# Kernel optimization log

Hardware: AMD Instinct MI355X
Metric: run time of the kernel (lower is better)

The kernel has to match this reference:

```python
import jax, jax.numpy as jnp
import numpy as np

N = 200_000
E = 3_200_000
H = 24

def setup_inputs() -> dict:
    key = jax.random.key(0)
    ks = jax.random.split(key, 12)
    s = 1.0 / np.sqrt(H).astype(np.float32)
    u = lambda k, shape: jax.random.uniform(k, shape, jnp.float32, -s, s)
    return {
        "x": jax.random.normal(ks[0], (N,), jnp.float32),
        "h0": jax.random.normal(ks[1], (1, N, H), jnp.float32) * 0.1,
        "c0": jax.random.normal(ks[2], (1, N, H), jnp.float32) * 0.1,
        "edge_index": jax.random.randint(ks[3], (2, E), 0, N, dtype=jnp.int32),
        "w_ih": u(ks[4], (4 * H, 1)),
        "w_hh": u(ks[5], (4 * H, H)),
        "b_ih": u(ks[6], (4 * H,)),
        "b_hh": u(ks[7], (4 * H,)),
        "gcn_w": u(ks[8], (H, H)),
        "gcn_b": u(ks[9], (H,)),
        "lin_w": u(ks[10], (1, H)),
        "lin_b": u(ks[11], (1,)),
    }

def reference(x, h0, c0, edge_index, w_ih, w_hh, b_ih, b_hh, gcn_w, gcn_b, lin_w, lin_b):
    # --- LSTM single step (seq_len=1, batch=N, input_size=1, hidden=H) ---
    h_prev = h0[0]  # [N, H]
    c_prev = c0[0]  # [N, H]
    # gates in torch order: input, forget, cell(g), output
    gates = x[:, None] * w_ih[:, 0][None, :] + b_ih + h_prev @ w_hh.T + b_hh  # [N, 4H]
    i, f, g, o = jnp.split(gates, 4, axis=-1)
    i = jax.nn.sigmoid(i); f = jax.nn.sigmoid(f); o = jax.nn.sigmoid(o); g = jnp.tanh(g)
    c = f * c_prev + i * g
    h = o * jnp.tanh(c)  # [N, H] -- LSTM output == new hidden state

    # --- GCNConv(24,24): symmetric norm with self loops (PyG default) ---
    xw = h @ gcn_w.T  # [N, H]
    src, dst = edge_index[0], edge_index[1]
    deg = jax.ops.segment_sum(jnp.ones(src.shape, xw.dtype), dst, num_segments=N) + 1.0
    dinv = jax.lax.rsqrt(deg)                      # deg >= 1 due to self loops
    norm = dinv[src] * dinv[dst]                   # [E]
    msg = xw[src] * norm[:, None]                  # [E, H]
    agg = jax.ops.segment_sum(msg, dst, num_segments=N)
    agg = agg + xw * (dinv * dinv)[:, None]        # self-loop edges
    conv = agg + gcn_b                             # [N, H]

    # --- Linear(24,1) + elementwise gate ---
    out = (conv @ lin_w.T + lin_b).reshape(-1)     # [N]
    return x * out, h[None], c[None]
```

## Files before the change

kernel.cpp:

```cpp
#include <hip/hip_runtime.h>
#include <math.h>

#define H 24
#define B0 4096
#define B0_SHIFT 12
#define MAXNB 64
#define NBPAD 65
#define P 20
#define CAP 70000
#define CSTRIDE 16
#define K1_EPB 4096

__device__ __forceinline__ float sigmoidf_(float v) {
    return 1.0f / (1.0f + __expf(-v));
}
__device__ __forceinline__ float tanhf_(float v) {
    return 1.0f - 2.0f / (__expf(2.0f * v) + 1.0f);
}

__global__ void init_kernel(unsigned* __restrict__ cursors,
                            const float* __restrict__ gcn_w,
                            const float* __restrict__ gcn_b,
                            const float* __restrict__ lin_w,
                            const float* __restrict__ lin_b,
                            float* __restrict__ g, float* __restrict__ cb, int NB) {
    int t = threadIdx.x;
    if (t < H) {
        float acc = 0.0f;
        for (int j = 0; j < H; j++) acc = fmaf(lin_w[j], gcn_w[j * H + t], acc);
        g[t] = acc;
    }
    if (t == 32) {
        float c = lin_b[0];
        for (int j = 0; j < H; j++) c = fmaf(gcn_b[j], lin_w[j], c);
        *cb = c;
    }
    if (t < MAXNB) cursors[t * CSTRIDE] = (unsigned)t * CAP;
}

__global__ __launch_bounds__(256) void scatter_kernel(
    const int* __restrict__ src, const int* __restrict__ dst,
    unsigned* __restrict__ cursors, unsigned* __restrict__ pedge, int E, int NB)
{
    __shared__ unsigned cnt[4][NBPAD];
    __shared__ unsigned c3[4][NBPAD];
    __shared__ unsigned base[4][NBPAD];

    const int tid = threadIdx.x;
    const int w = tid >> 6;
    const int start = blockIdx.x * K1_EPB;
    const bool full = (E - start) >= K1_EPB;
    const int ebase = start + tid * 16;

    for (int i = tid; i < 4 * NBPAD; i += 256) {
        (&cnt[0][0])[i] = 0;
        (&c3[0][0])[i] = 0;
    }
    __syncthreads();

    unsigned dreg[16];
    if (full) {
        const uint4* dp = (const uint4*)(dst + ebase);
        #pragma unroll
        for (int q = 0; q < 4; q++) {
            uint4 v = dp[q];
            dreg[4*q+0] = v.x; dreg[4*q+1] = v.y; dreg[4*q+2] = v.z; dreg[4*q+3] = v.w;
        }
        #pragma unroll
        for (int q = 0; q < 16; q++)
            atomicAdd(&cnt[w][dreg[q] >> B0_SHIFT], 1u);
    } else {
        #pragma unroll
        for (int q = 0; q < 16; q++) {
            int e = ebase + q;
            if (e < E) {
                unsigned d = (unsigned)dst[e];
                dreg[q] = d;
                atomicAdd(&cnt[w][d >> B0_SHIFT], 1u);
            } else dreg[q] = 0xFFFFFFFFu;
        }
    }
    __syncthreads();

    if (tid < NB) {
        unsigned c0 = cnt[0][tid], c1 = cnt[1][tid], c2 = cnt[2][tid], cw3 = cnt[3][tid];
        unsigned tot = c0 + c1 + c2 + cw3;
        unsigned gb = tot ? atomicAdd(&cursors[tid * CSTRIDE], tot) : 0u;
        base[0][tid] = gb;
        base[1][tid] = gb + c0;
        base[2][tid] = gb + c0 + c1;
        base[3][tid] = gb + c0 + c1 + c2;
    }
    __syncthreads();

    if (full) {
        unsigned sreg[16];
        const uint4* sp = (const uint4*)(src + ebase);
        #pragma unroll
        for (int q = 0; q < 4; q++) {
            uint4 v = sp[q];
            sreg[4*q+0] = v.x; sreg[4*q+1] = v.y; sreg[4*q+2] = v.z; sreg[4*q+3] = v.w;
        }
        #pragma unroll
        for (int q = 0; q < 16; q++) {
            unsigned d = dreg[q];
            unsigned b = d >> B0_SHIFT;
            unsigned slot = atomicAdd(&c3[w][b], 1u);
            unsigned idx  = base[w][b] + slot;
            if (idx < (b + 1u) * CAP)
                pedge[idx] = (sreg[q] << B0_SHIFT) | (d & (B0 - 1));
        }
    } else {
        #pragma unroll
        for (int q = 0; q < 16; q++) {
            int e = ebase + q;
            if (e < E) {
                unsigned d = dreg[q];
                unsigned b = d >> B0_SHIFT;
                unsigned slot = atomicAdd(&c3[w][b], 1u);
                unsigned idx  = base[w][b] + slot;
                if (idx < (b + 1u) * CAP)
                    pedge[idx] = ((unsigned)src[e] << B0_SHIFT) | (d & (B0 - 1));
            }
        }
    }
}

__global__ __launch_bounds__(256) void deghist_kernel(
    const unsigned* __restrict__ pedge, const unsigned* __restrict__ cursors,
    unsigned short* __restrict__ degp, int NB, int NPAD)
{
    __shared__ unsigned h[B0];
    int b = blockIdx.x % NB, p = blockIdx.x / NB;
    for (int i = threadIdx.x; i < B0; i += 256) h[i] = 0;
    __syncthreads();
    unsigned base = (unsigned)b * CAP;
    unsigned sz = cursors[b * CSTRIDE] - base; if (sz > CAP) sz = CAP;
    unsigned chunk = (sz + P - 1) / P;
    unsigned s0 = p * chunk;
    unsigned s1 = s0 + chunk; if (s1 > sz) s1 = sz;
    for (unsigned i = s0 + threadIdx.x; i < s1; i += 256)
        atomicAdd(&h[pedge[base + i] & (B0 - 1)], 1u);
    __syncthreads();
    unsigned short* out = degp + (size_t)p * NPAD + (size_t)b * B0;
    for (int i = threadIdx.x; i < B0; i += 256) out[i] = (unsigned short)h[i];
}

__global__ __launch_bounds__(256) void node_kernel(
    const float* __restrict__ x, const float* __restrict__ h0, const float* __restrict__ c0,
    const float* __restrict__ w_ih, const float* __restrict__ w_hh,
    const float* __restrict__ b_ih, const float* __restrict__ b_hh,
    const float* __restrict__ g,
    float* __restrict__ out_h, float* __restrict__ out_c,
    float* __restrict__ y, int N)
{
    __shared__ float ws[96 * 24];
    __shared__ float swih[96];
    __shared__ float sbs[96];
    __shared__ float sg[24];

    #pragma unroll 3
    for (int i = threadIdx.x; i < 96 * 24; i += 256) ws[i] = w_hh[i];
    if (threadIdx.x < 96) {
        swih[threadIdx.x] = w_ih[threadIdx.x];
        sbs[threadIdx.x]  = b_ih[threadIdx.x] + b_hh[threadIdx.x];
    } else if (threadIdx.x >= 128 && threadIdx.x < 152) {
        sg[threadIdx.x - 128] = g[threadIdx.x - 128];
    }
    __syncthreads();

    int tid = blockIdx.x * 256 + threadIdx.x;
    int pr  = tid >> 2;
    int n0  = pr * 2;
    if (n0 >= N) return;
    int n1  = n0 + 1;
    int t   = tid & 3;
    int k0  = 6 * t;

    float hp0[H], hp1[H];
    {
        const float4* a4 = (const float4*)(h0 + (size_t)n0 * H);
        const float4* b4 = (const float4*)(h0 + (size_t)n1 * H);
        #pragma unroll
        for (int q = 0; q < 6; q++) {
            float4 va = a4[q], vb = b4[q];
            hp0[4*q+0] = va.x; hp0[4*q+1] = va.y; hp0[4*q+2] = va.z; hp0[4*q+3] = va.w;
            hp1[4*q+0] = vb.x; hp1[4*q+1] = vb.y; hp1[4*q+2] = vb.z; hp1[4*q+3] = vb.w;
        }
    }
    float cp0[6], cp1[6];
    {
        const float2* a2 = (const float2*)(c0 + (size_t)n0 * H + k0);
        const float2* b2 = (const float2*)(c0 + (size_t)n1 * H + k0);
        #pragma unroll
        for (int q = 0; q < 3; q++) {
            float2 va = a2[q], vb = b2[q];
            cp0[2*q] = va.x; cp0[2*q+1] = va.y;
            cp1[2*q] = vb.x; cp1[2*q+1] = vb.y;
        }
    }
    float xv0 = x[n0], xv1 = x[n1];
    float yv0 = 0.0f, yv1 = 0.0f;

    #pragma unroll
    for (int i = 0; i < 6; i++) {
        int k = k0 + i;
        float bi = sbs[k], bf = sbs[k + 24], bg = sbs[k + 48], bo = sbs[k + 72];
        float wik = swih[k], wfk = swih[k + 24], wgk = swih[k + 48], wok = swih[k + 72];
        float gi0 = fmaf(xv0, wik, bi), gi1 = fmaf(xv1, wik, bi);
        float gf0 = fmaf(xv0, wfk, bf), gf1 = fmaf(xv1, wfk, bf);
        float gg0 = fmaf(xv0, wgk, bg), gg1 = fmaf(xv1, wgk, bg);
        float go0 = fmaf(xv0, wok, bo), go1 = fmaf(xv1, wok, bo);
        const float* w0 = ws + k * 24;
        #pragma unroll
        for (int c = 0; c < 6; c++) {
            float4 wi = *(const float4*)(w0 + 4*c);
            float4 wf = *(const float4*)(w0 + 576  + 4*c);
            float4 wg = *(const float4*)(w0 + 1152 + 4*c);
            float4 wo = *(const float4*)(w0 + 1728 + 4*c);
            float a0 = hp0[4*c+0], a1 = hp0[4*c+1], a2 = hp0[4*c+2], a3 = hp0[4*c+3];
            float d0 = hp1[4*c+0], d1 = hp1[4*c+1], d2 = hp1[4*c+2], d3 = hp1[4*c+3];
            gi0 = fmaf(a0, wi.x, gi0); gi0 = fmaf(a1, wi.y, gi0);
            gi0 = fmaf(a2, wi.z, gi0); gi0 = fmaf(a3, wi.w, gi0);
            gi1 = fmaf(d0, wi.x, gi1); gi1 = fmaf(d1, wi.y, gi1);
            gi1 = fmaf(d2, wi.z, gi1); gi1 = fmaf(d3, wi.w, gi1);
            gf0 = fmaf(a0, wf.x, gf0); gf0 = fmaf(a1, wf.y, gf0);
            gf0 = fmaf(a2, wf.z, gf0); gf0 = fmaf(a3, wf.w, gf0);
            gf1 = fmaf(d0, wf.x, gf1); gf1 = fmaf(d1, wf.y, gf1);
            gf1 = fmaf(d2, wf.z, gf1); gf1 = fmaf(d3, wf.w, gf1);
            gg0 = fmaf(a0, wg.x, gg0); gg0 = fmaf(a1, wg.y, gg0);
            gg0 = fmaf(a2, wg.z, gg0); gg0 = fmaf(a3, wg.w, gg0);
            gg1 = fmaf(d0, wg.x, gg1); gg1 = fmaf(d1, wg.y, gg1);
            gg1 = fmaf(d2, wg.z, gg1); gg1 = fmaf(d3, wg.w, gg1);
            go0 = fmaf(a0, wo.x, go0); go0 = fmaf(a1, wo.y, go0);
            go0 = fmaf(a2, wo.z, go0); go0 = fmaf(a3, wo.w, go0);
            go1 = fmaf(d0, wo.x, go1); go1 = fmaf(d1, wo.y, go1);
            go1 = fmaf(d2, wo.z, go1); go1 = fmaf(d3, wo.w, go1);
        }
        gi0 = sigmoidf_(gi0); gf0 = sigmoidf_(gf0); go0 = sigmoidf_(go0); gg0 = tanhf_(gg0);
        gi1 = sigmoidf_(gi1); gf1 = sigmoidf_(gf1); go1 = sigmoidf_(go1); gg1 = tanhf_(gg1);
        float c_0 = fmaf(gf0, cp0[i], gi0 * gg0);
        float c_1 = fmaf(gf1, cp1[i], gi1 * gg1);
        float h_0 = go0 * tanhf_(c_0);
        float h_1 = go1 * tanhf_(c_1);
        out_c[(size_t)n0 * H + k] = c_0;
        out_c[(size_t)n1 * H + k] = c_1;
        out_h[(size_t)n0 * H + k] = h_0;
        out_h[(size_t)n1 * H + k] = h_1;
        float gk = sg[k];
        yv0 = fmaf(h_0, gk, yv0);
        yv1 = fmaf(h_1, gk, yv1);
    }
    yv0 += __shfl_xor(yv0, 1); yv0 += __shfl_xor(yv0, 2);
    yv1 += __shfl_xor(yv1, 1); yv1 += __shfl_xor(yv1, 2);
    if (t == 0) y[n0] = yv0;
    if (t == 1) y[n1] = yv1;
}

__global__ __launch_bounds__(256) void z_kernel(
    const float* __restrict__ y, const unsigned short* __restrict__ degp, int NPAD,
    float* __restrict__ dinv, float* __restrict__ z, int N)
{
    int n = blockIdx.x * 256 + threadIdx.x;
    if (n >= N) return;
    unsigned dg = 0;
    #pragma unroll
    for (int p = 0; p < P; p++) dg += degp[(size_t)p * NPAD + n];
    float di = rsqrtf((float)dg + 1.0f);
    dinv[n] = di;
    z[n] = di * y[n];
}

__global__ __launch_bounds__(256) void acchist_kernel(
    const unsigned* __restrict__ pedge, const unsigned* __restrict__ cursors,
    const float* __restrict__ z, float* __restrict__ accp, int NB, int NPAD)
{
    __shared__ float h[B0];
    int b = blockIdx.x % NB, p = blockIdx.x / NB;
    for (int i = threadIdx.x; i < B0; i += 256) h[i] = 0.0f;
    __syncthreads();
    unsigned base = (unsigned)b * CAP;
    unsigned sz = cursors[b * CSTRIDE] - base; if (sz > CAP) sz = CAP;
    unsigned chunk = (sz + P - 1) / P;
    unsigned s0 = p * chunk;
    unsigned s1 = s0 + chunk; if (s1 > sz) s1 = sz;
    for (unsigned i = s0 + threadIdx.x; i < s1; i += 256) {
        unsigned v = pedge[base + i];
        atomicAdd(&h[v & (B0 - 1)], z[v >> B0_SHIFT]);
    }
    __syncthreads();
    float* out = accp + (size_t)p * NPAD + (size_t)b * B0;
    for (int i = threadIdx.x; i < B0; i += 256) out[i] = h[i];
}

__global__ __launch_bounds__(256) void final_kernel(
    const float* __restrict__ x, const float* __restrict__ accp, int NPAD,
    const float* __restrict__ y, const float* __restrict__ dinv,
    const float* __restrict__ cb, float* __restrict__ out, int N)
{
    int n = blockIdx.x * blockDim.x + threadIdx.x;
    if (n >= N) return;
    float a = 0.0f;
    #pragma unroll
    for (int p = 0; p < P; p++) a += accp[(size_t)p * NPAD + n];
    float di = dinv[n];
    float s  = di * a + di * di * y[n] + cb[0];
    out[n] = x[n] * s;
}

extern "C" void kernel_launch(void* const* d_in, const int* in_sizes, int n_in,
                              void* d_out, int out_size, void* d_ws, size_t ws_size,
                              hipStream_t stream) {
    const float* x     = (const float*)d_in[0];
    const float* h0    = (const float*)d_in[1];
    const float* c0    = (const float*)d_in[2];
    const int*   ei    = (const int*)d_in[3];
    const float* w_ih  = (const float*)d_in[4];
    const float* w_hh  = (const float*)d_in[5];
    const float* b_ih  = (const float*)d_in[6];
    const float* b_hh  = (const float*)d_in[7];
    const float* gcn_w = (const float*)d_in[8];
    const float* gcn_b = (const float*)d_in[9];
    const float* lin_w = (const float*)d_in[10];
    const float* lin_b = (const float*)d_in[11];

    const int N = in_sizes[0];
    const int E = in_sizes[3] / 2;
    const int* src = ei;
    const int* dst = ei + E;

    const int NB   = (N + B0 - 1) / B0;
    const int NPAD = NB * B0;

    float* out_gate = (float*)d_out;
    float* out_h    = out_gate + N;
    float* out_c    = out_h + (size_t)N * H;

    char* w = (char*)d_ws;
    unsigned*       pedge   = (unsigned*)w;       w += (size_t)NB * CAP * 4;
    unsigned short* degp    = (unsigned short*)w; w += (size_t)P * NPAD * 2;
    float*          accp    = (float*)w;          w += (size_t)P * NPAD * 4;
    float*          y       = (float*)w;          w += (size_t)N * 4;
    float*          zv      = (float*)w;          w += (size_t)N * 4;
    float*          dinv    = (float*)w;          w += (size_t)N * 4;
    float*          g       = (float*)w;          w += H * 4;
    float*          cb      = (float*)w;          w += 4;
    unsigned*       cursors = (unsigned*)w;       w += MAXNB * CSTRIDE * 4;

    init_kernel   <<<1, 64, 0, stream>>>(cursors, gcn_w, gcn_b, lin_w, lin_b, g, cb, NB);
    scatter_kernel<<<(E + K1_EPB - 1) / K1_EPB, 256, 0, stream>>>(src, dst, cursors,
                                                                  pedge, E, NB);
    deghist_kernel<<<NB * P, 256, 0, stream>>>(pedge, cursors, degp, NB, NPAD);
    node_kernel   <<<((size_t)N * 2 + 255) / 256, 256, 0, stream>>>(
                       x, h0, c0, w_ih, w_hh, b_ih, b_hh, g, out_h, out_c, y, N);
    z_kernel      <<<(N + 255) / 256, 256, 0, stream>>>(y, degp, NPAD, dinv, zv, N);
    acchist_kernel<<<NB * P, 256, 0, stream>>>(pedge, cursors, zv, accp, NB, NPAD);
    final_kernel  <<<(N + 255) / 256, 256, 0, stream>>>(x, accp, NPAD, y, dinv, cb,
                                                        out_gate, N);
}
```

Baseline: 110.0 us.

## Fuse z computation into node kernel and drop init kernel

Removes the init kernel by zeroing the cursors with hipMemsetAsync and storing bucket-relative offsets. The folded lin_w·gcn_w vector is now recomputed per block inside node_kernel, and the bias constant is recomputed per thread in final_kernel. The degree reduction and the z/dinv computation move from the separate z kernel into node_kernel's epilogue, which removes two launches and a reread of y. The cost is redundant small dot products in every block and thread, plus strided degp reads done by only two of every four lanes.

```diff
diff --git a/kernel.cpp b/kernel.cpp
--- a/kernel.cpp
+++ b/kernel.cpp
@@ -18,26 +18,6 @@
     return 1.0f - 2.0f / (__expf(2.0f * v) + 1.0f);
 }
 
-__global__ void init_kernel(unsigned* __restrict__ cursors,
-                            const float* __restrict__ gcn_w,
-                            const float* __restrict__ gcn_b,
-                            const float* __restrict__ lin_w,
-                            const float* __restrict__ lin_b,
-                            float* __restrict__ g, float* __restrict__ cb, int NB) {
-    int t = threadIdx.x;
-    if (t < H) {
-        float acc = 0.0f;
-        for (int j = 0; j < H; j++) acc = fmaf(lin_w[j], gcn_w[j * H + t], acc);
-        g[t] = acc;
-    }
-    if (t == 32) {
-        float c = lin_b[0];
-        for (int j = 0; j < H; j++) c = fmaf(gcn_b[j], lin_w[j], c);
-        *cb = c;
-    }
-    if (t < MAXNB) cursors[t * CSTRIDE] = (unsigned)t * CAP;
-}
-
 __global__ __launch_bounds__(256) void scatter_kernel(
     const int* __restrict__ src, const int* __restrict__ dst,
     unsigned* __restrict__ cursors, unsigned* __restrict__ pedge, int E, int NB)
@@ -106,9 +86,9 @@
             unsigned d = dreg[q];
             unsigned b = d >> B0_SHIFT;
             unsigned slot = atomicAdd(&c3[w][b], 1u);
-            unsigned idx  = base[w][b] + slot;
-            if (idx < (b + 1u) * CAP)
-                pedge[idx] = (sreg[q] << B0_SHIFT) | (d & (B0 - 1));
+            unsigned off  = base[w][b] + slot;
+            if (off < CAP)
+                pedge[(size_t)b * CAP + off] = (sreg[q] << B0_SHIFT) | (d & (B0 - 1));
         }
     } else {
         #pragma unroll
@@ -118,9 +98,9 @@
                 unsigned d = dreg[q];
                 unsigned b = d >> B0_SHIFT;
                 unsigned slot = atomicAdd(&c3[w][b], 1u);
-                unsigned idx  = base[w][b] + slot;
-                if (idx < (b + 1u) * CAP)
-                    pedge[idx] = ((unsigned)src[e] << B0_SHIFT) | (d & (B0 - 1));
+                unsigned off  = base[w][b] + slot;
+                if (off < CAP)
+                    pedge[(size_t)b * CAP + off] = ((unsigned)src[e] << B0_SHIFT) | (d & (B0 - 1));
             }
         }
     }
@@ -135,7 +115,7 @@
     for (int i = threadIdx.x; i < B0; i += 256) h[i] = 0;
     __syncthreads();
     unsigned base = (unsigned)b * CAP;
-    unsigned sz = cursors[b * CSTRIDE] - base; if (sz > CAP) sz = CAP;
+    unsigned sz = cursors[b * CSTRIDE]; if (sz > CAP) sz = CAP;
     unsigned chunk = (sz + P - 1) / P;
     unsigned s0 = p * chunk;
     unsigned s1 = s0 + chunk; if (s1 > sz) s1 = sz;
@@ -150,9 +130,10 @@
     const float* __restrict__ x, const float* __restrict__ h0, const float* __restrict__ c0,
     const float* __restrict__ w_ih, const float* __restrict__ w_hh,
     const float* __restrict__ b_ih, const float* __restrict__ b_hh,
-    const float* __restrict__ g,
+    const float* __restrict__ gcn_w, const float* __restrict__ lin_w,
+    const unsigned short* __restrict__ degp, int NPAD,
     float* __restrict__ out_h, float* __restrict__ out_c,
-    float* __restrict__ y, int N)
+    float* __restrict__ y, float* __restrict__ z, float* __restrict__ dinv, int N)
 {
     __shared__ float ws[96 * 24];
     __shared__ float swih[96];
@@ -165,7 +146,10 @@
         swih[threadIdx.x] = w_ih[threadIdx.x];
         sbs[threadIdx.x]  = b_ih[threadIdx.x] + b_hh[threadIdx.x];
     } else if (threadIdx.x >= 128 && threadIdx.x < 152) {
-        sg[threadIdx.x - 128] = g[threadIdx.x - 128];
+        int k = threadIdx.x - 128;
+        float acc = 0.0f;
+        for (int j = 0; j < H; j++) acc = fmaf(lin_w[j], gcn_w[j * H + k], acc);
+        sg[k] = acc;
     }
     __syncthreads();
 
@@ -253,22 +237,17 @@
     }
     yv0 += __shfl_xor(yv0, 1); yv0 += __shfl_xor(yv0, 2);
     yv1 += __shfl_xor(yv1, 1); yv1 += __shfl_xor(yv1, 2);
-    if (t == 0) y[n0] = yv0;
-    if (t == 1) y[n1] = yv1;
-}
-
-__global__ __launch_bounds__(256) void z_kernel(
-    const float* __restrict__ y, const unsigned short* __restrict__ degp, int NPAD,
-    float* __restrict__ dinv, float* __restrict__ z, int N)
-{
-    int n = blockIdx.x * 256 + threadIdx.x;
-    if (n >= N) return;
-    unsigned dg = 0;
-    #pragma unroll
-    for (int p = 0; p < P; p++) dg += degp[(size_t)p * NPAD + n];
-    float di = rsqrtf((float)dg + 1.0f);
-    dinv[n] = di;
-    z[n] = di * y[n];
+    if (t < 2) {
+        int n = (t == 0) ? n0 : n1;
+        float yv = (t == 0) ? yv0 : yv1;
+        unsigned dg = 0;
+        #pragma unroll
+        for (int p = 0; p < P; p++) dg += degp[(size_t)p * NPAD + n];
+        float di = rsqrtf((float)dg + 1.0f);
+        dinv[n] = di;
+        y[n] = yv;
+        z[n] = di * yv;
+    }
 }
 
 __global__ __launch_bounds__(256) void acchist_kernel(
@@ -280,7 +259,7 @@
     for (int i = threadIdx.x; i < B0; i += 256) h[i] = 0.0f;
     __syncthreads();
     unsigned base = (unsigned)b * CAP;
-    unsigned sz = cursors[b * CSTRIDE] - base; if (sz > CAP) sz = CAP;
+    unsigned sz = cursors[b * CSTRIDE]; if (sz > CAP) sz = CAP;
     unsigned chunk = (sz + P - 1) / P;
     unsigned s0 = p * chunk;
     unsigned s1 = s0 + chunk; if (s1 > sz) s1 = sz;
@@ -296,15 +275,19 @@
 __global__ __launch_bounds__(256) void final_kernel(
     const float* __restrict__ x, const float* __restrict__ accp, int NPAD,
     const float* __restrict__ y, const float* __restrict__ dinv,
-    const float* __restrict__ cb, float* __restrict__ out, int N)
+    const float* __restrict__ gcn_b, const float* __restrict__ lin_w,
+    const float* __restrict__ lin_b, float* __restrict__ out, int N)
 {
     int n = blockIdx.x * blockDim.x + threadIdx.x;
     if (n >= N) return;
+    float cb = lin_b[0];
+    #pragma unroll
+    for (int j = 0; j < H; j++) cb = fmaf(gcn_b[j], lin_w[j], cb);
     float a = 0.0f;
     #pragma unroll
     for (int p = 0; p < P; p++) a += accp[(size_t)p * NPAD + n];
     float di = dinv[n];
-    float s  = di * a + di * di * y[n] + cb[0];
+    float s  = di * a + di * di * y[n] + cb;
     out[n] = x[n] * s;
 }
 
@@ -343,18 +326,17 @@
     float*          y       = (float*)w;          w += (size_t)N * 4;
     float*          zv      = (float*)w;          w += (size_t)N * 4;
     float*          dinv    = (float*)w;          w += (size_t)N * 4;
-    float*          g       = (float*)w;          w += H * 4;
-    float*          cb      = (float*)w;          w += 4;
     unsigned*       cursors = (unsigned*)w;       w += MAXNB * CSTRIDE * 4;
 
-    init_kernel   <<<1, 64, 0, stream>>>(cursors, gcn_w, gcn_b, lin_w, lin_b, g, cb, NB);
+    hipMemsetAsync(cursors, 0, MAXNB * CSTRIDE * sizeof(unsigned), stream);
+
     scatter_kernel<<<(E + K1_EPB - 1) / K1_EPB, 256, 0, stream>>>(src, dst, cursors,
                                                                   pedge, E, NB);
     deghist_kernel<<<NB * P, 256, 0, stream>>>(pedge, cursors, degp, NB, NPAD);
     node_kernel   <<<((size_t)N * 2 + 255) / 256, 256, 0, stream>>>(
-                       x, h0, c0, w_ih, w_hh, b_ih, b_hh, g, out_h, out_c, y, N);
-    z_kernel      <<<(N + 255) / 256, 256, 0, stream>>>(y, degp, NPAD, dinv, zv, N);
+                       x, h0, c0, w_ih, w_hh, b_ih, b_hh, gcn_w, lin_w, degp, NPAD,
+                       out_h, out_c, y, zv, dinv, N);
     acchist_kernel<<<NB * P, 256, 0, stream>>>(pedge, cursors, zv, accp, NB, NPAD);
-    final_kernel  <<<(N + 255) / 256, 256, 0, stream>>>(x, accp, NPAD, y, dinv, cb,
-                                                        out_gate, N);
-}
+    final_kernel  <<<(N + 255) / 256, 256, 0, stream>>>(x, accp, NPAD, y, dinv,
+                                                        gcn_b, lin_w, lin_b, out_gate, N);
+}
```

Measured after the change: 108.2 us. Within noise of the previous version (-1.6%).
